# Kernel optimization log

Measured on AMD Instinct MI355X. Metric: run time of the kernel, lower is better.

Reference implementation:

```python
import jax, jax.numpy as jnp
import numpy as np

HEADS = 8
DIM_HEAD = 40
LN_EPS = 1e-5


def setup_inputs() -> dict:
    key = jax.random.key(0)
    ks = jax.random.split(key, 6)
    b, c, h, w = 8, 320, 64, 64
    ctx_len, ctx_dim = 77, 768
    inner = HEADS * DIM_HEAD  # 320
    return {
        "x": jax.random.normal(ks[0], (b, c, h, w), jnp.float32),
        "context": jax.random.normal(ks[1], (b, ctx_len, ctx_dim), jnp.float32),
        "Wq": jax.random.normal(ks[2], (c, inner), jnp.float32) * 0.02,
        "Wk": jax.random.normal(ks[3], (ctx_dim, inner), jnp.float32) * 0.02,
        "Wv": jax.random.normal(ks[4], (ctx_dim, inner), jnp.float32) * 0.02,
        "Wout": jax.random.normal(ks[5], (inner, c), jnp.float32) * 0.02,
        "bout": jnp.zeros((c,), jnp.float32),
        "gamma": jnp.ones((c,), jnp.float32),
        "beta": jnp.zeros((c,), jnp.float32),
    }


def reference(x, context, Wq, Wk, Wv, Wout, bout, gamma, beta):
    b, c, h, w = x.shape
    n = h * w
    scale = DIM_HEAD ** -0.5
    # flatten spatial -> tokens: [b, n, c]
    x_flat = x.reshape(b, c, n).transpose(0, 2, 1)
    # LayerNorm over channel dim
    mu = jnp.mean(x_flat, axis=-1, keepdims=True)
    var = jnp.mean((x_flat - mu) ** 2, axis=-1, keepdims=True)
    x_norm = (x_flat - mu) / jnp.sqrt(var + LN_EPS) * gamma + beta
    # projections (no bias), split heads: [b, h, n, d]
    def split_heads(t):
        bb, nn, _ = t.shape
        return t.reshape(bb, nn, HEADS, DIM_HEAD).transpose(0, 2, 1, 3)
    q = split_heads(x_norm @ Wq)
    k = split_heads(context @ Wk)
    v = split_heads(context @ Wv)
    sim = jnp.einsum("bhid,bhjd->bhij", q, k) * scale  # [b,H,n,ctx]
    attn = jax.nn.softmax(sim, axis=-1)
    out = jnp.einsum("bhij,bhjd->bhid", attn, v)
    out = out.transpose(0, 2, 1, 3).reshape(b, n, HEADS * DIM_HEAD)
    out = out @ Wout + bout  # dropout is identity at inference
    out = out + x_flat
    return out.transpose(0, 2, 1).reshape(b, c, h, w)
```

## Files before the change

kernel.cpp:

```cpp
#include <hip/hip_runtime.h>

#define HEADS 8
#define DH 40
constexpr int Bn   = 8;
constexpr int Cc   = 320;
constexpr int Nn   = 4096;
constexpr int CTX  = 77;
constexpr float LN_EPS = 1e-5f;
constexpr float SCALE  = 0.15811388300841897f;

typedef short bf16x8 __attribute__((ext_vector_type(8)));
typedef float f32x4  __attribute__((ext_vector_type(4)));
typedef unsigned short us;

__device__ inline us f2bf(float f) {
    unsigned u = __float_as_uint(f);
    u += 0x7fffu + ((u >> 16) & 1u);
    return (us)(u >> 16);
}
__device__ inline float bf2f(us h) {
    return __uint_as_float(((unsigned)h) << 16);
}

__global__ __launch_bounds__(256) void wtrans_all(const float* __restrict__ Wq,
                                                  const float* __restrict__ Wk,
                                                  const float* __restrict__ Wv,
                                                  const float* __restrict__ Wout,
                                                  us* __restrict__ wqF,
                                                  us* __restrict__ WkT,
                                                  us* __restrict__ WvT,
                                                  us* __restrict__ WoutT) {
    int id = blockIdx.x;
    if (id >= 580) {
        int wid = (id - 580) * 4 + (threadIdx.x >> 6);
        int lane = threadIdx.x & 63, lr = lane & 15, g = lane >> 4;
        int ct = wid / 10, kc = wid % 10;
        int k0 = kc * 32 + g * 8, co = ct * 16 + lr;
        us tmp[8];
        #pragma unroll
        for (int e = 0; e < 8; ++e)
            tmp[e] = f2bf(Wq[(size_t)(k0 + e) * 320 + co]);
        ((uint4*)wqF)[(size_t)wid * 64 + lane] = *(uint4*)tmp;
        return;
    }
    const float* in; us* out; int K, t;
    if (id < 240)      { in = Wk;   out = WkT;   K = 768; t = id; }
    else if (id < 480) { in = Wv;   out = WvT;   K = 768; t = id - 240; }
    else               { in = Wout; out = WoutT; K = 320; t = id - 480; }
    int ktiles = K >> 5;
    int kb = (t % ktiles) * 32, ob = (t / ktiles) * 32;

    __shared__ float tile[32][33];
    int tx = threadIdx.x & 31, ty = threadIdx.x >> 5;
    #pragma unroll
    for (int i = 0; i < 32; i += 8)
        tile[ty + i][tx] = in[(size_t)(kb + ty + i) * 320 + ob + tx];
    __syncthreads();
    #pragma unroll
    for (int i = 0; i < 32; i += 8)
        out[(size_t)(ob + ty + i) * K + kb + tx] = f2bf(tile[tx][ty + i]);
}

__global__ __launch_bounds__(256, 3) void ln_q_fused(const float* __restrict__ x,
                                                     const float* __restrict__ gamma,
                                                     const float* __restrict__ beta,
                                                     const us* __restrict__ wqF,
                                                     us* __restrict__ qG) {
    __shared__ __align__(16) us xnt[64 * 328];
    __shared__ float red1[4][64], red2[4][64];
    __shared__ float mu_s[64], rs_s[64];

    int b  = blockIdx.x >> 6;
    int t0 = (blockIdx.x & 63) * 64;
    int tid = threadIdx.x;
    int tl = tid & 63, cg = tid >> 6;
    const float* xb = x + (size_t)b * Cc * Nn + t0 + tl;

    float s1 = 0.f, s2 = 0.f;
    #pragma unroll 8
    for (int i = 0; i < 80; ++i) {
        int c = cg * 80 + i;
        float v = xb[(size_t)c * Nn];
        s1 += v; s2 += v * v;
        xnt[tl * 328 + c] = f2bf(v);
    }
    red1[cg][tl] = s1; red2[cg][tl] = s2;
    __syncthreads();
    if (tid < 64) {
        float a1 = red1[0][tl] + red1[1][tl] + red1[2][tl] + red1[3][tl];
        float a2 = red2[0][tl] + red2[1][tl] + red2[2][tl] + red2[3][tl];
        float mu = a1 * (1.0f / Cc);
        float var = a2 * (1.0f / Cc) - mu * mu;
        mu_s[tl] = mu; rs_s[tl] = rsqrtf(var + LN_EPS);
    }
    __syncthreads();
    float mu = mu_s[tl], rs = rs_s[tl];
    #pragma unroll 4
    for (int i = 0; i < 40; ++i) {
        int c = cg * 80 + i * 2;
        unsigned u = *(unsigned*)&xnt[tl * 328 + c];
        float v0 = bf2f((us)(u & 0xffff));
        float v1 = bf2f((us)(u >> 16));
        unsigned lo = f2bf((v0 - mu) * rs * gamma[c]     + beta[c]);
        unsigned hi = f2bf((v1 - mu) * rs * gamma[c + 1] + beta[c + 1]);
        *(unsigned*)&xnt[tl * 328 + c] = lo | (hi << 16);
    }
    __syncthreads();

    int lane = tid & 63, w = tid >> 6;
    int lr = lane & 15, g = lane >> 4;
    f32x4 acc[4][5] = {};
    const bf16x8* wq = (const bf16x8*)wqF;
    for (int kc = 0; kc < 10; ++kc) {
        bf16x8 bfr[5];
        #pragma unroll
        for (int nt = 0; nt < 5; ++nt)
            bfr[nt] = wq[(size_t)((w * 5 + nt) * 10 + kc) * 64 + lane];
        bf16x8 afr[4];
        #pragma unroll
        for (int mt = 0; mt < 4; ++mt)
            afr[mt] = *(const bf16x8*)&xnt[(mt * 16 + lr) * 328 + kc * 32 + g * 8];
        #pragma unroll
        for (int mt = 0; mt < 4; ++mt)
            #pragma unroll
            for (int nt = 0; nt < 5; ++nt)
                acc[mt][nt] = __builtin_amdgcn_mfma_f32_16x16x32_bf16(afr[mt], bfr[nt], acc[mt][nt], 0, 0, 0);
    }
    __syncthreads();

    #pragma unroll
    for (int mt = 0; mt < 4; ++mt)
        #pragma unroll
        for (int nt = 0; nt < 5; ++nt)
            #pragma unroll
            for (int r = 0; r < 4; ++r)
                xnt[(mt * 16 + g * 4 + r) * 328 + w * 80 + nt * 16 + lr] = f2bf(acc[mt][nt][r]);
    __syncthreads();

    size_t gtb = (size_t)b * 256 + (blockIdx.x & 63) * 4;
    #pragma unroll
    for (int it = 0; it < 10; ++it) {
        int f_lin = it * 4 + w;
        int tile = f_lin / 10, f = f_lin % 10;
        uint4 v = *(uint4*)&xnt[(tile * 16 + lr) * 328 + f * 32 + g * 8];
        ((uint4*)qG)[((gtb + tile) * 10 + f) * 64 + lane] = v;
    }
}

__global__ __launch_bounds__(256) void gemm_kv(const float* __restrict__ ctx,
                                               const us* __restrict__ WkT,
                                               const us* __restrict__ WvT,
                                               us* __restrict__ kbuf,
                                               us* __restrict__ vbuf) {
    const us* Bt = blockIdx.z ? WvT : WkT;
    us* Cm = blockIdx.z ? vbuf : kbuf;
    constexpr int K = 768, M = 616;
    __shared__ __align__(16) char Al[64 * 128];
    __shared__ __align__(16) char Bl[64 * 128];
    int m0 = blockIdx.x * 64;
    int n0 = blockIdx.y * 64;
    int tid = threadIdx.x;
    int lane = tid & 63, wave = tid >> 6;
    int wm = (wave >> 1) * 32, wn = (wave & 1) * 32;

    f32x4 acc[2][2] = {};

    for (int kc = 0; kc < K; kc += 64) {
        #pragma unroll
        for (int i = 0; i < 2; ++i) {
            int chunk = tid + 256 * i;
            int r = chunk >> 3, c8 = chunk & 7;
            int off = (r * 128 + c8 * 16) ^ ((r & 7) << 4);
            int gr = m0 + r;
            uint4 av = make_uint4(0, 0, 0, 0);
            if (gr < M) {
                float4 f0 = *(const float4*)(ctx + (size_t)gr * K + kc + c8 * 8);
                float4 f1 = *(const float4*)(ctx + (size_t)gr * K + kc + c8 * 8 + 4);
                av.x = f2bf(f0.x) | ((unsigned)f2bf(f0.y) << 16);
                av.y = f2bf(f0.z) | ((unsigned)f2bf(f0.w) << 16);
                av.z = f2bf(f1.x) | ((unsigned)f2bf(f1.y) << 16);
                av.w = f2bf(f1.z) | ((unsigned)f2bf(f1.w) << 16);
            }
            *(uint4*)(Al + off) = av;
            *(uint4*)(Bl + off) = *(const uint4*)(Bt + (size_t)(n0 + r) * K + kc + c8 * 8);
        }
        __syncthreads();

        #pragma unroll
        for (int kk = 0; kk < 64; kk += 32) {
            bf16x8 a[2], bfr[2];
            int lr = lane & 15;
            int lkb = (kk + (lane >> 4) * 8) * 2;
            #pragma unroll
            for (int mi = 0; mi < 2; ++mi) {
                int row = wm + mi * 16 + lr;
                a[mi] = *(const bf16x8*)(Al + ((row * 128 + lkb) ^ ((row & 7) << 4)));
            }
            #pragma unroll
            for (int ni = 0; ni < 2; ++ni) {
                int row = wn + ni * 16 + lr;
                bfr[ni] = *(const bf16x8*)(Bl + ((row * 128 + lkb) ^ ((row & 7) << 4)));
            }
            #pragma unroll
            for (int mi = 0; mi < 2; ++mi)
                #pragma unroll
                for (int ni = 0; ni < 2; ++ni)
                    acc[mi][ni] = __builtin_amdgcn_mfma_f32_16x16x32_bf16(a[mi], bfr[ni], acc[mi][ni], 0, 0, 0);
        }
        __syncthreads();
    }

    int lr = lane & 15, lq = lane >> 4;
    #pragma unroll
    for (int mi = 0; mi < 2; ++mi)
        #pragma unroll
        for (int ni = 0; ni < 2; ++ni)
            #pragma unroll
            for (int r = 0; r < 4; ++r) {
                int row = m0 + wm + mi * 16 + lq * 4 + r;
                int col = n0 + wn + ni * 16 + lr;
                if (row < M)
                    Cm[(size_t)row * 320 + col] = f2bf(acc[mi][ni][r]);
            }
}

__global__ __launch_bounds__(256) void gemm_vw(const us* __restrict__ WoutT,
                                               const us* __restrict__ vbuf,
                                               us* __restrict__ vwT) {
    int b = blockIdx.z, h = blockIdx.y, cb = blockIdx.x * 64;
    int tid = threadIdx.x, lane = tid & 63, w = tid >> 6;
    int lr = lane & 15, g = lane >> 4;

    int crow = cb + w * 16 + lr;
    const us* ab = WoutT + (size_t)crow * 320 + h * DH;
    bf16x8 a0 = *(const bf16x8*)(ab + g * 8);
    bf16x8 a1 = {};
    if (g == 0) a1 = *(const bf16x8*)(ab + 32);

    f32x4 acc[5] = {};
    #pragma unroll
    for (int nt = 0; nt < 5; ++nt) {
        int j = nt * 16 + lr;
        bool jv = j < CTX;
        const us* kr = vbuf + (size_t)(b * CTX + (jv ? j : 0)) * 320 + h * DH;
        bf16x8 b0 = {}, b1 = {};
        if (jv) b0 = *(const bf16x8*)(kr + g * 8);
        if (jv && g == 0) b1 = *(const bf16x8*)(kr + 32);
        acc[nt] = __builtin_amdgcn_mfma_f32_16x16x32_bf16(a0, b0, acc[nt], 0, 0, 0);
        acc[nt] = __builtin_amdgcn_mfma_f32_16x16x32_bf16(a1, b1, acc[nt], 0, 0, 0);
    }

    #pragma unroll
    for (int nt = 0; nt < 5; ++nt)
        #pragma unroll
        for (int r = 0; r < 4; ++r) {
            int c = cb + w * 16 + g * 4 + r;
            float val = (nt == 4 && lr >= 13) ? 0.f : acc[nt][r];
            vwT[((size_t)(b * 320 + c)) * 640 + h * 80 + nt * 16 + lr] = f2bf(val);
        }
}

__global__ __launch_bounds__(256) void repack_all(const us* __restrict__ kbuf,
                                                  const us* __restrict__ vwT,
                                                  us* __restrict__ kF,
                                                  us* __restrict__ vwF) {
    int id = blockIdx.x;
    int lane = threadIdx.x & 63, lr = lane & 15, g = lane >> 4;
    if (id < 160) {
        int wid = id * 4 + (threadIdx.x >> 6);
        int kc = wid & 1, nt = (wid >> 1) % 5, h = (wid / 10) & 7, b = wid / 80;
        int j = nt * 16 + lr, d0 = kc * 32 + g * 8;
        bf16x8 v = {};
        if (j < CTX && d0 < DH)
            v = *(const bf16x8*)(kbuf + ((size_t)(b * CTX + j)) * 320 + h * DH + d0);
        ((bf16x8*)kF)[(size_t)wid * 64 + lane] = v;
    } else {
        int wid = (id - 160) * 4 + (threadIdx.x >> 6);
        int mi = wid % 5, ks = (wid / 5) % 20, w = (wid / 100) & 3, b = wid / 400;
        int co = w * 80 + mi * 16 + lr, k = ks * 32 + g * 8;
        bf16x8 v = *(const bf16x8*)(vwT + ((size_t)(b * 320 + co)) * 640 + k);
        ((bf16x8*)vwF)[(size_t)wid * 64 + lane] = v;
    }
}

__global__ __launch_bounds__(512, 4) void attn_out(const us* __restrict__ qG,
                                                   const us* __restrict__ kF,
                                                   const us* __restrict__ vwF,
                                                   const float* __restrict__ bout,
                                                   const float* __restrict__ x,
                                                   float* __restrict__ out) {
    __shared__ __align__(16) char Pl[64 * 1280];

    int bid = blockIdx.x;
    int b = bid & 7, ts = bid >> 3;
    int t0 = ts * 64;
    int tid = threadIdx.x, lane = tid & 63, w = tid >> 6;
    int lr = lane & 15, g = lane >> 4;

    const bf16x8* qfb = (const bf16x8*)qG;
    const bf16x8* kfb = (const bf16x8*)kF;

    {
        int h = w;
        size_t kfh = (size_t)((b * 8 + h) * 10) * 64;
        bf16x8 kb0[5], kb1[5];
        #pragma unroll
        for (int nt = 0; nt < 5; ++nt) {
            kb0[nt] = kfb[kfh + (nt * 2 + 0) * 64 + lane];
            kb1[nt] = kfb[kfh + (nt * 2 + 1) * 64 + lane];
        }
        int f0 = (5 * h + g) >> 2, l0 = ((5 * h + g) & 3) * 16 + lr;
        int f1 = (5 * h + 4) >> 2, l1 = ((5 * h + 4) & 3) * 16 + lr;

        #pragma unroll
        for (int mt = 0; mt < 4; ++mt) {
            const bf16x8* qt = qfb + (size_t)(b * 256 + ts * 4 + mt) * 640;
            bf16x8 a0 = qt[f0 * 64 + l0];
            bf16x8 a1 = {};
            if (g == 0) a1 = qt[f1 * 64 + l1];

            f32x4 S[5] = {};
            #pragma unroll
            for (int nt = 0; nt < 5; ++nt) {
                S[nt] = __builtin_amdgcn_mfma_f32_16x16x32_bf16(a0, kb0[nt], S[nt], 0, 0, 0);
                S[nt] = __builtin_amdgcn_mfma_f32_16x16x32_bf16(a1, kb1[nt], S[nt], 0, 0, 0);
            }

            float pv[5][4];
            #pragma unroll
            for (int nt = 0; nt < 5; ++nt)
                #pragma unroll
                for (int r = 0; r < 4; ++r)
                    pv[nt][r] = (nt == 4 && lr >= 13) ? 0.f : __expf(S[nt][r] * SCALE);
            #pragma unroll
            for (int r = 0; r < 4; ++r) {
                float su = pv[0][r] + pv[1][r] + pv[2][r] + pv[3][r] + pv[4][r];
                #pragma unroll
                for (int off = 1; off < 16; off <<= 1)
                    su += __shfl_xor(su, off);
                float inv = 1.0f / su;
                int row = mt * 16 + g * 4 + r;
                #pragma unroll
                for (int nt = 0; nt < 5; ++nt)
                    *(us*)(Pl + ((row * 1280 + (h * 80 + nt * 16 + lr) * 2) ^ ((row & 7) << 4))) =
                        f2bf(pv[nt][r] * inv);
            }
        }
    }
    __syncthreads();

    int wc = w >> 1, wt = w & 1;
    f32x4 o[5][2] = {};
    const bf16x8* vwb = (const bf16x8*)vwF + (size_t)((b * 4 + wc) * 100) * 64 + lane;
    __builtin_amdgcn_s_setprio(1);
    for (int ks = 0; ks < 20; ++ks) {
        bf16x8 av[5];
        #pragma unroll
        for (int mi = 0; mi < 5; ++mi)
            av[mi] = vwb[(ks * 5 + mi) * 64];
        bf16x8 pb[2];
        #pragma unroll
        for (int nt = 0; nt < 2; ++nt) {
            int row = wt * 32 + nt * 16 + lr;
            pb[nt] = *(const bf16x8*)(Pl + ((row * 1280 + ks * 64 + g * 16) ^ ((row & 7) << 4)));
        }
        #pragma unroll
        for (int mi = 0; mi < 5; ++mi)
            #pragma unroll
            for (int nt = 0; nt < 2; ++nt)
                o[mi][nt] = __builtin_amdgcn_mfma_f32_16x16x32_bf16(av[mi], pb[nt], o[mi][nt], 0, 0, 0);
    }
    __builtin_amdgcn_s_setprio(0);

    int cw = wc * 80;
    #pragma unroll
    for (int mi = 0; mi < 5; ++mi)
        #pragma unroll
        for (int r = 0; r < 4; ++r) {
            int co = cw + mi * 16 + g * 4 + r;
            float bo = bout[co];
            #pragma unroll
            for (int nt = 0; nt < 2; ++nt) {
                size_t oi = ((size_t)(b * 320 + co)) * 4096 + t0 + wt * 32 + nt * 16 + lr;
                out[oi] = o[mi][nt][r] + bo + x[oi];
            }
        }
}

extern "C" void kernel_launch(void* const* d_in, const int* in_sizes, int n_in,
                              void* d_out, int out_size, void* d_ws, size_t ws_size,
                              hipStream_t stream) {
    const float* x     = (const float*)d_in[0];
    const float* ctx   = (const float*)d_in[1];
    const float* Wq    = (const float*)d_in[2];
    const float* Wk    = (const float*)d_in[3];
    const float* Wv    = (const float*)d_in[4];
    const float* Wout  = (const float*)d_in[5];
    const float* bout  = (const float*)d_in[6];
    const float* gamma = (const float*)d_in[7];
    const float* beta  = (const float*)d_in[8];
    float* out = (float*)d_out;
    char* ws = (char*)d_ws;

    us* qG    = (us*)(ws);
    us* kbuf  = (us*)(ws + 20971520);
    us* vbuf  = (us*)(ws + 21365760);
    us* vwT   = (us*)(ws + 21760000);
    us* vwF   = (us*)(ws + 25036800);
    us* kF    = (us*)(ws + 28313600);
    us* wqF   = (us*)(ws + 28968960);
    us* WkT   = (us*)(ws + 29173760);
    us* WvT   = (us*)(ws + 29665280);
    us* WoutT = (us*)(ws + 30156800);

    wtrans_all<<<dim3(630), 256, 0, stream>>>(Wq, Wk, Wv, Wout, wqF, WkT, WvT, WoutT);
    gemm_kv<<<dim3(10, 5, 2), 256, 0, stream>>>(ctx, WkT, WvT, kbuf, vbuf);
    gemm_vw<<<dim3(5, 8, 8), 256, 0, stream>>>(WoutT, vbuf, vwT);
    repack_all<<<dim3(960), 256, 0, stream>>>(kbuf, vwT, kF, vwF);
    ln_q_fused<<<dim3(512), 256, 0, stream>>>(x, gamma, beta, wqF, qG);
    attn_out<<<dim3(512), 512, 0, stream>>>(qG, kF, vwF, bout, x, out);
}
```

Measured before the change: 91.66 us.

## Fuse LayerNorm+Q projection into attention kernel, keep Q in LDS

Merges the LayerNorm/Q-projection kernel into the attention/out-projection kernel, so Q stays in shared memory and no longer makes a bf16 round trip through global memory (about 20 MB). The x tile is kept in registers from the LayerNorm pass and reused for the residual add. The epilogue is staged through LDS so output stores and x reads are coalesced along tokens. In exchange the kernel uses about 124 KB of LDS and more registers, with launch bounds cut to 2 blocks per CU, which lowers occupancy.

After: 120.0 us. 30.9% more time.

```diff
diff --git a/kernel.cpp b/kernel.cpp
--- a/kernel.cpp
+++ b/kernel.cpp
@@ -17,9 +17,6 @@
     unsigned u = __float_as_uint(f);
     u += 0x7fffu + ((u >> 16) & 1u);
     return (us)(u >> 16);
-}
-__device__ inline float bf2f(us h) {
-    return __uint_as_float(((unsigned)h) << 16);
 }
 
 __global__ __launch_bounds__(256) void wtrans_all(const float* __restrict__ Wq,
@@ -59,92 +56,6 @@
     #pragma unroll
     for (int i = 0; i < 32; i += 8)
         out[(size_t)(ob + ty + i) * K + kb + tx] = f2bf(tile[tx][ty + i]);
-}
-
-__global__ __launch_bounds__(256, 3) void ln_q_fused(const float* __restrict__ x,
-                                                     const float* __restrict__ gamma,
-                                                     const float* __restrict__ beta,
-                                                     const us* __restrict__ wqF,
-                                                     us* __restrict__ qG) {
-    __shared__ __align__(16) us xnt[64 * 328];
-    __shared__ float red1[4][64], red2[4][64];
-    __shared__ float mu_s[64], rs_s[64];
-
-    int b  = blockIdx.x >> 6;
-    int t0 = (blockIdx.x & 63) * 64;
-    int tid = threadIdx.x;
-    int tl = tid & 63, cg = tid >> 6;
-    const float* xb = x + (size_t)b * Cc * Nn + t0 + tl;
-
-    float s1 = 0.f, s2 = 0.f;
-    #pragma unroll 8
-    for (int i = 0; i < 80; ++i) {
-        int c = cg * 80 + i;
-        float v = xb[(size_t)c * Nn];
-        s1 += v; s2 += v * v;
-        xnt[tl * 328 + c] = f2bf(v);
-    }
-    red1[cg][tl] = s1; red2[cg][tl] = s2;
-    __syncthreads();
-    if (tid < 64) {
-        float a1 = red1[0][tl] + red1[1][tl] + red1[2][tl] + red1[3][tl];
-        float a2 = red2[0][tl] + red2[1][tl] + red2[2][tl] + red2[3][tl];
-        float mu = a1 * (1.0f / Cc);
-        float var = a2 * (1.0f / Cc) - mu * mu;
-        mu_s[tl] = mu; rs_s[tl] = rsqrtf(var + LN_EPS);
-    }
-    __syncthreads();
-    float mu = mu_s[tl], rs = rs_s[tl];
-    #pragma unroll 4
-    for (int i = 0; i < 40; ++i) {
-        int c = cg * 80 + i * 2;
-        unsigned u = *(unsigned*)&xnt[tl * 328 + c];
-        float v0 = bf2f((us)(u & 0xffff));
-        float v1 = bf2f((us)(u >> 16));
-        unsigned lo = f2bf((v0 - mu) * rs * gamma[c]     + beta[c]);
-        unsigned hi = f2bf((v1 - mu) * rs * gamma[c + 1] + beta[c + 1]);
-        *(unsigned*)&xnt[tl * 328 + c] = lo | (hi << 16);
-    }
-    __syncthreads();
-
-    int lane = tid & 63, w = tid >> 6;
-    int lr = lane & 15, g = lane >> 4;
-    f32x4 acc[4][5] = {};
-    const bf16x8* wq = (const bf16x8*)wqF;
-    for (int kc = 0; kc < 10; ++kc) {
-        bf16x8 bfr[5];
-        #pragma unroll
-        for (int nt = 0; nt < 5; ++nt)
-            bfr[nt] = wq[(size_t)((w * 5 + nt) * 10 + kc) * 64 + lane];
-        bf16x8 afr[4];
-        #pragma unroll
-        for (int mt = 0; mt < 4; ++mt)
-            afr[mt] = *(const bf16x8*)&xnt[(mt * 16 + lr) * 328 + kc * 32 + g * 8];
-        #pragma unroll
-        for (int mt = 0; mt < 4; ++mt)
-            #pragma unroll
-            for (int nt = 0; nt < 5; ++nt)
-                acc[mt][nt] = __builtin_amdgcn_mfma_f32_16x16x32_bf16(afr[mt], bfr[nt], acc[mt][nt], 0, 0, 0);
-    }
-    __syncthreads();
-
-    #pragma unroll
-    for (int mt = 0; mt < 4; ++mt)
-        #pragma unroll
-        for (int nt = 0; nt < 5; ++nt)
-            #pragma unroll
-            for (int r = 0; r < 4; ++r)
-                xnt[(mt * 16 + g * 4 + r) * 328 + w * 80 + nt * 16 + lr] = f2bf(acc[mt][nt][r]);
-    __syncthreads();
-
-    size_t gtb = (size_t)b * 256 + (blockIdx.x & 63) * 4;
-    #pragma unroll
-    for (int it = 0; it < 10; ++it) {
-        int f_lin = it * 4 + w;
-        int tile = f_lin / 10, f = f_lin % 10;
-        uint4 v = *(uint4*)&xnt[(tile * 16 + lr) * 328 + f * 32 + g * 8];
-        ((uint4*)qG)[((gtb + tile) * 10 + f) * 64 + lane] = v;
-    }
 }
 
 __global__ __launch_bounds__(256) void gemm_kv(const float* __restrict__ ctx,
@@ -283,23 +194,83 @@
     }
 }
 
-__global__ __launch_bounds__(512, 4) void attn_out(const us* __restrict__ qG,
-                                                   const us* __restrict__ kF,
-                                                   const us* __restrict__ vwF,
-                                                   const float* __restrict__ bout,
-                                                   const float* __restrict__ x,
-                                                   float* __restrict__ out) {
-    __shared__ __align__(16) char Pl[64 * 1280];
+__global__ __launch_bounds__(512, 2) void fused_ln_attn(const float* __restrict__ x,
+                                                        const float* __restrict__ gamma,
+                                                        const float* __restrict__ beta,
+                                                        const us* __restrict__ wqF,
+                                                        const us* __restrict__ kF,
+                                                        const us* __restrict__ vwF,
+                                                        const float* __restrict__ bout,
+                                                        float* __restrict__ out) {
+    __shared__ __align__(16) char smem[123904];
+    __shared__ float red1[8][64], red2[8][64];
+    __shared__ float mu_s[64], rs_s[64];
+    __shared__ float bo_s[320];
+
+    us*    qlds = (us*)smem;
+    char*  Pl   = smem + 41984;
+    float* epi  = (float*)smem;
 
     int bid = blockIdx.x;
     int b = bid & 7, ts = bid >> 3;
     int t0 = ts * 64;
-    int tid = threadIdx.x, lane = tid & 63, w = tid >> 6;
+    int tid = threadIdx.x;
+    int tl = tid & 63, cg = tid >> 6;
+    int lane = tid & 63, w = cg;
     int lr = lane & 15, g = lane >> 4;
 
-    const bf16x8* qfb = (const bf16x8*)qG;
+    if (tid < 320) bo_s[tid] = bout[tid];
+
+    const float* xb = x + ((size_t)b * Cc) * Nn + t0 + tl;
+    float xr[40];
+    float s1 = 0.f, s2 = 0.f;
+    #pragma unroll
+    for (int i = 0; i < 40; ++i) {
+        float v = xb[(size_t)(cg * 40 + i) * Nn];
+        xr[i] = v; s1 += v; s2 += v * v;
+    }
+    red1[cg][tl] = s1; red2[cg][tl] = s2;
+    __syncthreads();
+    if (tid < 64) {
+        float a1 = 0.f, a2 = 0.f;
+        #pragma unroll
+        for (int k = 0; k < 8; ++k) { a1 += red1[k][tl]; a2 += red2[k][tl]; }
+        float muv = a1 * (1.0f / Cc);
+        float var = a2 * (1.0f / Cc) - muv * muv;
+        mu_s[tl] = muv; rs_s[tl] = rsqrtf(var + LN_EPS);
+    }
+    __syncthreads();
+
+    float mu = mu_s[tl], rs = rs_s[tl];
+    #pragma unroll
+    for (int i = 0; i < 20; ++i) {
+        int c = cg * 40 + i * 2;
+        unsigned lo = f2bf((xr[i * 2]     - mu) * rs * gamma[c]     + beta[c]);
+        unsigned hi = f2bf((xr[i * 2 + 1] - mu) * rs * gamma[c + 1] + beta[c + 1]);
+        *(unsigned*)&qlds[tl * 328 + c] = lo | (hi << 16);
+    }
+    __syncthreads();
+
+    int mt = w & 3, ch = w >> 2;
+    f32x4 acc[10] = {};
+    const bf16x8* wq = (const bf16x8*)wqF;
+    for (int kc = 0; kc < 10; ++kc) {
+        bf16x8 afr = *(const bf16x8*)&qlds[(mt * 16 + lr) * 328 + kc * 32 + g * 8];
+        #pragma unroll
+        for (int nt2 = 0; nt2 < 10; ++nt2) {
+            bf16x8 bfr = wq[(size_t)((ch * 10 + nt2) * 10 + kc) * 64 + lane];
+            acc[nt2] = __builtin_amdgcn_mfma_f32_16x16x32_bf16(afr, bfr, acc[nt2], 0, 0, 0);
+        }
+    }
+    __syncthreads();
+    #pragma unroll
+    for (int nt2 = 0; nt2 < 10; ++nt2)
+        #pragma unroll
+        for (int r = 0; r < 4; ++r)
+            qlds[(mt * 16 + g * 4 + r) * 328 + ch * 160 + nt2 * 16 + lr] = f2bf(acc[nt2][r]);
+    __syncthreads();
+
     const bf16x8* kfb = (const bf16x8*)kF;
-
     {
         int h = w;
         size_t kfh = (size_t)((b * 8 + h) * 10) * 64;
@@ -309,15 +280,11 @@
             kb0[nt] = kfb[kfh + (nt * 2 + 0) * 64 + lane];
             kb1[nt] = kfb[kfh + (nt * 2 + 1) * 64 + lane];
         }
-        int f0 = (5 * h + g) >> 2, l0 = ((5 * h + g) & 3) * 16 + lr;
-        int f1 = (5 * h + 4) >> 2, l1 = ((5 * h + 4) & 3) * 16 + lr;
-
-        #pragma unroll
-        for (int mt = 0; mt < 4; ++mt) {
-            const bf16x8* qt = qfb + (size_t)(b * 256 + ts * 4 + mt) * 640;
-            bf16x8 a0 = qt[f0 * 64 + l0];
+        #pragma unroll
+        for (int mt2 = 0; mt2 < 4; ++mt2) {
+            bf16x8 a0 = *(const bf16x8*)&qlds[(mt2 * 16 + lr) * 328 + h * 40 + g * 8];
             bf16x8 a1 = {};
-            if (g == 0) a1 = qt[f1 * 64 + l1];
+            if (g == 0) a1 = *(const bf16x8*)&qlds[(mt2 * 16 + lr) * 328 + h * 40 + 32];
 
             f32x4 S[5] = {};
             #pragma unroll
@@ -339,7 +306,7 @@
                 for (int off = 1; off < 16; off <<= 1)
                     su += __shfl_xor(su, off);
                 float inv = 1.0f / su;
-                int row = mt * 16 + g * 4 + r;
+                int row = mt2 * 16 + g * 4 + r;
                 #pragma unroll
                 for (int nt = 0; nt < 5; ++nt)
                     *(us*)(Pl + ((row * 1280 + (h * 80 + nt * 16 + lr) * 2) ^ ((row & 7) << 4))) =
@@ -371,20 +338,27 @@
                 o[mi][nt] = __builtin_amdgcn_mfma_f32_16x16x32_bf16(av[mi], pb[nt], o[mi][nt], 0, 0, 0);
     }
     __builtin_amdgcn_s_setprio(0);
-
-    int cw = wc * 80;
+    __syncthreads();
+
     #pragma unroll
     for (int mi = 0; mi < 5; ++mi)
         #pragma unroll
         for (int r = 0; r < 4; ++r) {
-            int co = cw + mi * 16 + g * 4 + r;
-            float bo = bout[co];
+            int co = wc * 80 + mi * 16 + g * 4 + r;
+            float bo = bo_s[co];
             #pragma unroll
             for (int nt = 0; nt < 2; ++nt) {
-                size_t oi = ((size_t)(b * 320 + co)) * 4096 + t0 + wt * 32 + nt * 16 + lr;
-                out[oi] = o[mi][nt][r] + bo + x[oi];
-            }
-        }
+                int tok = wt * 32 + nt * 16 + lr;
+                epi[tok * 329 + co] = o[mi][nt][r] + bo;
+            }
+        }
+    __syncthreads();
+
+    #pragma unroll
+    for (int i = 0; i < 40; ++i) {
+        int c = cg * 40 + i;
+        out[((size_t)(b * 320 + c)) * 4096 + t0 + tl] = epi[tl * 329 + c] + xr[i];
+    }
 }
 
 extern "C" void kernel_launch(void* const* d_in, const int* in_sizes, int n_in,
@@ -402,21 +376,19 @@
     float* out = (float*)d_out;
     char* ws = (char*)d_ws;
 
-    us* qG    = (us*)(ws);
-    us* kbuf  = (us*)(ws + 20971520);
-    us* vbuf  = (us*)(ws + 21365760);
-    us* vwT   = (us*)(ws + 21760000);
-    us* vwF   = (us*)(ws + 25036800);
-    us* kF    = (us*)(ws + 28313600);
-    us* wqF   = (us*)(ws + 28968960);
-    us* WkT   = (us*)(ws + 29173760);
-    us* WvT   = (us*)(ws + 29665280);
-    us* WoutT = (us*)(ws + 30156800);
+    us* kbuf  = (us*)(ws);
+    us* vbuf  = (us*)(ws + 394240);
+    us* vwT   = (us*)(ws + 788480);
+    us* vwF   = (us*)(ws + 4065280);
+    us* kF    = (us*)(ws + 7342080);
+    us* wqF   = (us*)(ws + 7997440);
+    us* WkT   = (us*)(ws + 8202240);
+    us* WvT   = (us*)(ws + 8693760);
+    us* WoutT = (us*)(ws + 9185280);
 
     wtrans_all<<<dim3(630), 256, 0, stream>>>(Wq, Wk, Wv, Wout, wqF, WkT, WvT, WoutT);
     gemm_kv<<<dim3(10, 5, 2), 256, 0, stream>>>(ctx, WkT, WvT, kbuf, vbuf);
     gemm_vw<<<dim3(5, 8, 8), 256, 0, stream>>>(WoutT, vbuf, vwT);
     repack_all<<<dim3(960), 256, 0, stream>>>(kbuf, vwT, kF, vwF);
-    ln_q_fused<<<dim3(512), 256, 0, stream>>>(x, gamma, beta, wqF, qG);
-    attn_out<<<dim3(512), 512, 0, stream>>>(qG, kF, vwF, bout, x, out);
-}
+    fused_ln_attn<<<dim3(512), 512, 0, stream>>>(x, gamma, beta, wqF, kF, vwF, bout, out);
+}
```
